# Performance work log

Measured on AMD Instinct MI355X. Metric: run time of the kernel, lower is better.

Reference implementation:

```python
import jax, jax.numpy as jnp
import numpy as np

B, N, DIM, H, DH, K = 4, 2048, 512, 6, 64, 16
KEEP_PROB = 0.9  # 1 - dropout_rate
LOG2PI = float(np.log(2.0 * np.pi))
LOG_PRIOR = float(np.log(1.0 / K))


def setup_inputs() -> dict:
    key = jax.random.key(0)
    ks = jax.random.split(key, 7)
    inputs_q = jax.random.normal(ks[0], (B, N, DIM), dtype=jnp.float32)
    # decoder-style causal mask, shape [B, 1, q_len, kv_len]
    causal = jnp.tril(jnp.ones((N, N), dtype=jnp.float32))
    mask = jnp.broadcast_to(causal[None, None], (B, 1, N, N))
    # dropout keep mask broadcast across the query dim: [B, H, 1, kv_len]
    keep = jax.random.bernoulli(ks[1], KEEP_PROB, (B, H, 1, N)).astype(jnp.float32)
    w_qkv = jax.random.normal(ks[2], (DIM, 3 * H * DH), dtype=jnp.float32) * 0.02
    w_out = jax.random.normal(ks[3], (H * DH, DIM), dtype=jnp.float32) * 0.02
    mu_lookup = jax.random.normal(ks[4], (K, DIM), dtype=jnp.float32)
    logvar_lookup = jax.random.normal(ks[5], (K, DIM), dtype=jnp.float32) * 0.1
    return {
        "inputs_q": inputs_q,
        "mask": mask,
        "keep": keep,
        "w_qkv": w_qkv,
        "w_out": w_out,
        "mu_lookup": mu_lookup,
        "logvar_lookup": logvar_lookup,
    }


def reference(inputs_q, mask, keep, w_qkv, w_out, mu_lookup, logvar_lookup):
    # --- MultiHeadDotProductAttention (self-attn path) ---
    qkv = (inputs_q @ w_qkv).reshape(B, N, 3, H, DH)  # [B,N,3,H,DH]
    q, k, v = qkv[:, :, 0], qkv[:, :, 1], qkv[:, :, 2]
    # bias: 0 where mask > 0, -1e10 elsewhere (note: no 1/sqrt(d) scaling, as in source)
    bias = jnp.where(mask > 0, 0.0, -1e10)
    attn_weights = jnp.einsum('bqhd,bkhd->bhqk', q, k) + bias  # [B,H,N,N]
    attn_weights = jax.nn.softmax(attn_weights, axis=-1)
    # broadcast dropout: mask shared across the query dim
    attn_weights = attn_weights * keep / KEEP_PROB
    attn_out = jnp.einsum('bhqk,bkhd->bqhd', attn_weights, v)
    attn_out = attn_out.reshape(B, N, H * DH) @ w_out  # [B,N,DIM]

    # --- GMM posterior approx q(y|x) ~= p(y|z) (approx_qy_x, vectorized over k) ---
    z = attn_out.mean(axis=1)  # pooled latent, [B,DIM]
    diff = z[:, None, :] - mu_lookup[None]  # [B,K,DIM]
    llh = -0.5 * jnp.sum(
        diff * diff / jnp.exp(logvar_lookup)[None] + logvar_lookup[None] + LOG2PI,
        axis=-1,
    )  # [B,K]
    logLogit_qy_x = llh + LOG_PRIOR
    qy_x = jax.nn.softmax(logLogit_qy_x, axis=1)  # [B,K]

    # combine mixture mean back in so both branches are live in one output
    return attn_out + (qy_x @ mu_lookup)[:, None, :]
```

## Files before the change

### kernel.cpp

```cpp
#include <hip/hip_runtime.h>
#include <cstdint>
#include <cstddef>

#define NH 6
#define NSEQ 2048
#define DIMD 512
#define BATCH 4
#define HD 384
#define LOG2PI_F 1.8378770664093453f

typedef __attribute__((ext_vector_type(8))) short short8;
typedef __attribute__((ext_vector_type(8))) unsigned short ushort8;
typedef __attribute__((ext_vector_type(4))) unsigned short ushort4v;
typedef __attribute__((ext_vector_type(4))) float floatx4;

__device__ inline unsigned short f2bf(float f){
  unsigned int u = __float_as_uint(f);
  u += 0x7FFFu + ((u>>16)&1u);
  return (unsigned short)(u>>16);
}

#define GLD16(gp, lp) __builtin_amdgcn_global_load_lds( \
  (const __attribute__((address_space(1))) void*)(gp), \
  (__attribute__((address_space(3))) void*)(lp), 16, 0, 0)

__global__ __launch_bounds__(256) void convert_x(
    const float* __restrict__ xq, unsigned short* __restrict__ xbf)
{
  int i = blockIdx.x*256 + threadIdx.x;
  floatx4 v = *(const floatx4*)(xq + (size_t)i*4);
  ushort4v r;
  #pragma unroll
  for(int j=0;j<4;j++) r[j] = f2bf(v[j]);
  *(ushort4v*)(xbf + (size_t)i*4) = r;
}

__global__ __launch_bounds__(256) void wtrans(
    const float* __restrict__ src, unsigned short* __restrict__ dst, int R, int C)
{
  __shared__ __attribute__((aligned(16))) unsigned short Ls[64*72];
  const int t = threadIdx.x;
  const int r = t>>2, c0 = (t&3)*16;
  const int d0 = blockIdx.y*64, n0 = blockIdx.x*64;
  #pragma unroll
  for (int j=0;j<16;j+=4){
    floatx4 v = *(const floatx4*)(src + (size_t)(d0+r)*C + n0 + c0 + j);
    #pragma unroll
    for(int jj=0;jj<4;jj++) Ls[r*72 + c0+j+jj] = f2bf(v[jj]);
  }
  __syncthreads();
  #pragma unroll
  for (int j=0;j<16;j+=8){
    ushort8 o;
    #pragma unroll
    for(int jj=0;jj<8;jj++) o[jj] = Ls[(c0+j+jj)*72 + r];
    *(ushort8*)(dst + (size_t)(n0+r)*R + d0 + c0 + j) = o;
  }
}

__global__ __launch_bounds__(256) void vtrans(
    const unsigned short* __restrict__ Vo, unsigned short* __restrict__ Vt)
{
  __shared__ __attribute__((aligned(16))) unsigned short Ls[64*72];
  const int t = threadIdx.x;
  const int r = t>>2, c0 = (t&3)*16;
  const int n0 = blockIdx.x*64, bh = blockIdx.y;
  #pragma unroll
  for (int j=0;j<16;j+=8)
    *(ushort8*)(Ls + r*72 + c0 + j) = *(const ushort8*)(Vo + ((size_t)bh*NSEQ + n0 + r)*64 + c0 + j);
  __syncthreads();
  #pragma unroll
  for (int j=0;j<16;j+=8){
    ushort8 o;
    #pragma unroll
    for(int jj=0;jj<8;jj++) o[jj] = Ls[(c0+j+jj)*72 + r];
    *(ushort8*)(Vt + ((size_t)bh*64 + r)*NSEQ + n0 + c0 + j) = o;
  }
}

__global__ __launch_bounds__(256) void gemm_qkv(
    const unsigned short* __restrict__ A,
    const unsigned short* __restrict__ Bt,
    const float* __restrict__ keep,
    unsigned short* __restrict__ Qo, unsigned short* __restrict__ Ko, unsigned short* __restrict__ Vo)
{
  __shared__ __attribute__((aligned(16))) unsigned short Cs[128*132];
  unsigned short* As = Cs;
  unsigned short* Bs = Cs + 128*64;
  const int tid = threadIdx.x;
  const int w = tid>>6, lane = tid&63;
  const int wr = w>>1, wc = w&1;
  const int quad = lane>>4, l16 = lane&15;
  const int tM = blockIdx.x*128, tN = blockIdx.y*128;
  const int r8 = lane>>3, c8 = (lane&7)*8;
  floatx4 acc[4][4];
  floatx4 zed = {0.f,0.f,0.f,0.f};
  #pragma unroll
  for (int i=0;i<4;i++)
    #pragma unroll
    for(int j=0;j<4;j++) acc[i][j] = zed;

  for (int k0=0; k0<512; k0+=64){
    #pragma unroll
    for (int i=0;i<4;i++){
      int row = w*32 + i*8;
      GLD16(A  + (size_t)(tM+row+r8)*512 + k0 + c8, As + row*64);
      GLD16(Bt + (size_t)(tN+row+r8)*512 + k0 + c8, Bs + row*64);
    }
    __syncthreads();
    #pragma unroll
    for (int kk=0; kk<64; kk+=32){
      short8 af[4], bf[4];
      #pragma unroll
      for(int mt=0;mt<4;mt++)
        af[mt] = *(const short8*)(As + (wr*64+mt*16+l16)*64 + kk + quad*8);
      #pragma unroll
      for(int nt=0;nt<4;nt++)
        bf[nt] = *(const short8*)(Bs + (wc*64+nt*16+l16)*64 + kk + quad*8);
      #pragma unroll
      for(int mt=0;mt<4;mt++)
        #pragma unroll
        for(int nt=0;nt<4;nt++)
          acc[mt][nt] = __builtin_amdgcn_mfma_f32_16x16x32_bf16(af[mt], bf[nt], acc[mt][nt], 0,0,0);
    }
    __syncthreads();
  }
  #pragma unroll
  for(int mt=0;mt<4;mt++)
    #pragma unroll
    for(int nt=0;nt<4;nt++)
      #pragma unroll
      for(int r=0;r<4;r++)
        Cs[(wr*64+mt*16+quad*4+r)*132 + wc*64+nt*16+l16] = f2bf(acc[mt][nt][r]);
  __syncthreads();
  const int row = tid>>1, colh = (tid&1)*64;
  const int gcol0 = tN + colh;
  const int t = gcol0/384, rem = gcol0 - t*384, h = rem>>6;
  const int grow = tM + row, b = grow>>11, n = grow & 2047;
  unsigned short* dst = (t==0 ? Qo : (t==1 ? Ko : Vo)) + ((size_t)((b*NH+h)*NSEQ+n))*64;
  bool vzero = false;
  if (t==2) vzero = (keep[(size_t)(b*NH+h)*NSEQ+n] < 0.5f);
  ushort8 zz;
  #pragma unroll
  for(int q2=0;q2<8;q2++) zz[q2]=0;
  #pragma unroll
  for(int j=0;j<8;j++){
    ushort8 v = *(const ushort8*)(Cs + row*132 + colh + j*8);
    *(ushort8*)(dst + j*8) = vzero ? zz : v;
  }
}

__global__ __launch_bounds__(64) void attn_kernel(
    const unsigned short* __restrict__ Qg, const unsigned short* __restrict__ Kg,
    const unsigned short* __restrict__ VtG,
    unsigned short* __restrict__ atp)
{
  __shared__ __attribute__((aligned(16))) unsigned short Ps[32*72];
  const int lane = threadIdx.x;
  const int quad = lane>>4, l16 = lane&15;
  const int bid = blockIdx.x;
  const int idx = bid>>3;
  const int bh  = (bid&7) + 8*(idx % 3);
  const int c   = 63 - idx/3;
  const int b = bh/NH, h = bh - b*NH;
  const unsigned short* Qb = Qg  + (size_t)bh*NSEQ*64;
  const unsigned short* Kb = Kg  + (size_t)bh*NSEQ*64;
  const unsigned short* Vb = VtG + (size_t)bh*64*NSEQ;
  const int q0 = c*32;
  const int nkt = (c>>1) + 1;

  short8 qf[2][2];
  #pragma unroll
  for(int mt=0;mt<2;mt++)
    #pragma unroll
    for(int kc=0;kc<2;kc++)
      qf[mt][kc] = *(const short8*)(Qb + (size_t)(q0+mt*16+l16)*64 + kc*32 + quad*8);

  short8 onesf;
  #pragma unroll
  for(int j=0;j<8;j++) onesf[j] = (short)0x3F80;

  floatx4 O[2][4];
  floatx4 accl[2];
  floatx4 zed = {0.f,0.f,0.f,0.f};
  #pragma unroll
  for(int mt=0;mt<2;mt++){
    #pragma unroll
    for(int dt=0;dt<4;dt++) O[mt][dt] = zed;
    accl[mt] = zed;
  }

  short8 kA[4][2], kB2[4][2];
  auto loadK = [&](int kt, short8 (&kf)[4][2]){
    const unsigned short* kp0 = Kb + (size_t)kt*64*64;
    #pragma unroll
    for(int nt=0;nt<4;nt++)
      #pragma unroll
      for(int kc=0;kc<2;kc++)
        kf[nt][kc] = *(const short8*)(kp0 + (size_t)(nt*16+l16)*64 + kc*32 + quad*8);
  };

  auto tile = [&](int kt, short8 (&kf)[4][2]){
    const int kB = kt*64;
    short8 vf[2][4];
    const unsigned short* vp0 = Vb + kB;
    #pragma unroll
    for(int kh=0;kh<2;kh++)
      #pragma unroll
      for(int dt=0;dt<4;dt++)
        vf[kh][dt] = *(const short8*)(vp0 + (size_t)(dt*16+l16)*NSEQ + kh*32 + quad*8);

    floatx4 sacc[2][4];
    floatx4 m12 = {-12.f,-12.f,-12.f,-12.f};
    #pragma unroll
    for(int mt=0;mt<2;mt++)
      #pragma unroll
      for(int nt=0;nt<4;nt++) sacc[mt][nt] = m12;
    #pragma unroll
    for(int mt=0;mt<2;mt++)
      #pragma unroll
      for(int nt=0;nt<4;nt++)
        #pragma unroll
        for(int kc=0;kc<2;kc++)
          sacc[mt][nt] = __builtin_amdgcn_mfma_f32_16x16x32_bf16(qf[mt][kc], kf[nt][kc], sacc[mt][nt], 0,0,0);

    const bool dia = (kt == nkt-1);
    #pragma unroll
    for(int mt=0;mt<2;mt++){
      #pragma unroll
      for(int nt=0;nt<4;nt++){
        int key = kB + nt*16 + l16;
        #pragma unroll
        for(int r=0;r<4;r++){
          float p = __expf(sacc[mt][nt][r]);
          if (dia) p = (key <= q0 + mt*16 + quad*4 + r) ? p : 0.f;
          Ps[(mt*16+quad*4+r)*72 + nt*16 + l16] = f2bf(p);
        }
      }
    }
    #pragma unroll
    for(int kh=0;kh<2;kh++){
      #pragma unroll
      for(int mt=0;mt<2;mt++){
        short8 pf = *(const short8*)(Ps + (mt*16+l16)*72 + kh*32 + quad*8);
        accl[mt] = __builtin_amdgcn_mfma_f32_16x16x32_bf16(pf, onesf, accl[mt], 0,0,0);
        #pragma unroll
        for(int dt=0;dt<4;dt++)
          O[mt][dt] = __builtin_amdgcn_mfma_f32_16x16x32_bf16(pf, vf[kh][dt], O[mt][dt], 0,0,0);
      }
    }
  };

  loadK(0, kA);
  int kt = 0;
  while (true){
    loadK(kt+1 < nkt ? kt+1 : kt, kB2);
    tile(kt, kA);
    kt++; if (kt >= nkt) break;
    loadK(kt+1 < nkt ? kt+1 : kt, kA);
    tile(kt, kB2);
    kt++; if (kt >= nkt) break;
  }

  #pragma unroll
  for(int mt=0;mt<2;mt++)
    #pragma unroll
    for(int r=0;r<4;r++){
      float sc2 = (1.0f/0.9f) / accl[mt][r];
      #pragma unroll
      for(int dt=0;dt<4;dt++)
        Ps[(mt*16+quad*4+r)*72 + dt*16 + l16] = f2bf(O[mt][dt][r]*sc2);
    }
  const int orow = lane>>1, ohalf = (lane&1)*32;
  const int q = q0 + orow;
  unsigned short* dstp = atp + ((size_t)(b*NSEQ+q))*HD + h*64 + ohalf;
  #pragma unroll
  for(int j=0;j<4;j++)
    *(ushort8*)(dstp + j*8) = *(const ushort8*)(Ps + orow*72 + ohalf + j*8);
}

__global__ __launch_bounds__(256) void gemm_proj(
    const unsigned short* __restrict__ A,
    const unsigned short* __restrict__ Bt,
    float* __restrict__ out,
    float* __restrict__ z)
{
  __shared__ __attribute__((aligned(16))) unsigned short As[128*64];
  __shared__ __attribute__((aligned(16))) unsigned short Bs[128*64];
  const int tid = threadIdx.x;
  const int w = tid>>6, lane = tid&63;
  const int wr = w>>1, wc = w&1;
  const int quad = lane>>4, l16 = lane&15;
  const int tM = blockIdx.x*128, tN = blockIdx.y*128;
  const int r8 = lane>>3, c8 = (lane&7)*8;
  floatx4 acc[4][4];
  floatx4 zed = {0.f,0.f,0.f,0.f};
  #pragma unroll
  for (int i=0;i<4;i++)
    #pragma unroll
    for(int j=0;j<4;j++) acc[i][j] = zed;

  for (int k0=0; k0<384; k0+=64){
    #pragma unroll
    for (int i=0;i<4;i++){
      int row = w*32 + i*8;
      GLD16(A  + (size_t)(tM+row+r8)*384 + k0 + c8, As + row*64);
      GLD16(Bt + (size_t)(tN+row+r8)*384 + k0 + c8, Bs + row*64);
    }
    __syncthreads();
    #pragma unroll
    for (int kk=0; kk<64; kk+=32){
      short8 af[4], bf[4];
      #pragma unroll
      for(int mt=0;mt<4;mt++)
        af[mt] = *(const short8*)(As + (wr*64+mt*16+l16)*64 + kk + quad*8);
      #pragma unroll
      for(int nt=0;nt<4;nt++)
        bf[nt] = *(const short8*)(Bs + (wc*64+nt*16+l16)*64 + kk + quad*8);
      #pragma unroll
      for(int mt=0;mt<4;mt++)
        #pragma unroll
        for(int nt=0;nt<4;nt++)
          acc[mt][nt] = __builtin_amdgcn_mfma_f32_16x16x32_bf16(af[mt], bf[nt], acc[mt][nt], 0,0,0);
    }
    __syncthreads();
  }
  #pragma unroll
  for(int mt=0;mt<4;mt++){
    int grow = tM + wr*64 + mt*16 + quad*4;
    #pragma unroll
    for(int nt=0;nt<4;nt++){
      int gcol = tN + wc*64 + nt*16 + l16;
      #pragma unroll
      for(int r=0;r<4;r++)
        out[(size_t)(grow+r)*512 + gcol] = acc[mt][nt][r];
    }
  }
  #pragma unroll
  for(int nt=0;nt<4;nt++){
    float s = 0.f;
    #pragma unroll
    for(int mt=0;mt<4;mt++)
      #pragma unroll
      for(int r=0;r<4;r++) s += acc[mt][nt][r];
    s += __shfl_xor(s, 16, 64);
    s += __shfl_xor(s, 32, 64);
    if (quad == 0){
      int gcol = tN + wc*64 + nt*16 + l16;
      atomicAdd(&z[(tM>>11)*DIMD + gcol], s);
    }
  }
}

__global__ __launch_bounds__(256) void gmm_kernel(
    const float* __restrict__ z, const float* __restrict__ mu,
    const float* __restrict__ lv, float* __restrict__ c)
{
  __shared__ float sh[16];
  __shared__ float qy[16];
  int tid = threadIdx.x;
  int k = tid>>4, li = tid&15;
  int b = blockIdx.x;
  float part = 0.f;
  for(int d=li; d<DIMD; d+=16){
    float zz = z[b*DIMD+d] * (1.0f/2048.0f);
    float m = mu[k*DIMD+d], l = lv[k*DIMD+d];
    float diff = zz - m;
    part += diff*diff*__expf(-l) + l + LOG2PI_F;
  }
  #pragma unroll
  for(int off=8;off>=1;off>>=1) part += __shfl_xor(part, off, 64);
  if (li==0) sh[k] = part;
  __syncthreads();
  if (tid<16){
    float logit = -0.5f*sh[tid];
    float mx = logit;
    #pragma unroll
    for(int off=8;off>=1;off>>=1) mx = fmaxf(mx, __shfl_xor(mx, off, 64));
    float e = __expf(logit-mx);
    float se = e;
    #pragma unroll
    for(int off=8;off>=1;off>>=1) se += __shfl_xor(se, off, 64);
    qy[tid] = e/se;
  }
  __syncthreads();
  for(int d=tid; d<DIMD; d+=256){
    float accv = 0.f;
    #pragma unroll
    for(int kk=0;kk<16;kk++) accv += qy[kk]*mu[kk*DIMD+d];
    c[b*DIMD+d] = accv;
  }
}

__global__ __launch_bounds__(256) void final_add(
    float* __restrict__ out, const float* __restrict__ c)
{
  size_t i = ((size_t)blockIdx.x*256 + threadIdx.x)*4;
  int d = (int)(i & 511);
  int b = (int)(i >> 20);
  floatx4 a = *(const floatx4*)(out + i);
  floatx4 cc = *(const floatx4*)(c + b*DIMD + d);
  *(floatx4*)(out + i) = a + cc;
}

extern "C" void kernel_launch(void* const* d_in, const int* in_sizes, int n_in,
                              void* d_out, int out_size, void* d_ws, size_t ws_size,
                              hipStream_t stream) {
  const float* inputs_q = (const float*)d_in[0];
  const float* keep  = (const float*)d_in[2];
  const float* w_qkv = (const float*)d_in[3];
  const float* w_out = (const float*)d_in[4];
  const float* mu    = (const float*)d_in[5];
  const float* lv    = (const float*)d_in[6];
  float* out = (float*)d_out;
  char* ws = (char*)d_ws;
  size_t off = 0;
  auto alloc = [&](size_t bytes){ void* p = ws + off; off += (bytes + 255) & ~(size_t)255; return p; };
  unsigned short* Qb  = (unsigned short*)alloc((size_t)24*2048*64*2);
  unsigned short* Kb  = (unsigned short*)alloc((size_t)24*2048*64*2);
  unsigned short* Vo  = (unsigned short*)alloc((size_t)24*2048*64*2);
  unsigned short* Vt  = (unsigned short*)alloc((size_t)24*64*2048*2);
  unsigned short* xbf = (unsigned short*)alloc((size_t)8192*512*2);
  unsigned short* wqT = (unsigned short*)alloc((size_t)1152*512*2);
  unsigned short* woT = (unsigned short*)alloc((size_t)512*384*2);
  unsigned short* atp = (unsigned short*)alloc((size_t)8192*384*2);
  float* z  = (float*)alloc((size_t)4*512*4);
  float* c  = (float*)alloc((size_t)4*512*4);

  hipMemsetAsync(z, 0, 4*512*4, stream);
  convert_x<<<4096, 256, 0, stream>>>(inputs_q, xbf);
  wtrans<<<dim3(18,8), 256, 0, stream>>>(w_qkv, wqT, 512, 1152);
  wtrans<<<dim3(8,6),  256, 0, stream>>>(w_out, woT, 384, 512);
  gemm_qkv<<<dim3(64,9), 256, 0, stream>>>(xbf, wqT, keep, Qb, Kb, Vo);
  vtrans<<<dim3(32,24), 256, 0, stream>>>(Vo, Vt);
  attn_kernel<<<1536, 64, 0, stream>>>(Qb, Kb, Vt, atp);
  gemm_proj<<<dim3(64,4), 256, 0, stream>>>(atp, woT, out, z);
  gmm_kernel<<<4, 256, 0, stream>>>(z, mu, lv, c);
  final_add<<<4096, 256, 0, stream>>>(out, c);
}
```

Measured before the change: 246.1 us.

## Split attention key tiles across four waves and reduce partial outputs in LDS

The attention kernel now runs four waves per block, each handling every fourth key tile for the same 32-query block. Per-wave partial O and row-sum accumulators are written to shared memory and summed before normalisation and the bf16 store. This shortens the serial key loop of each block for long causal rows and improves load balance. In exchange it adds an LDS reduction, two barriers and larger shared memory, and short rows leave some waves idle.

Result: slower. 265.8 us (+8.0%).

```diff
diff --git a/kernel.cpp b/kernel.cpp
--- a/kernel.cpp
+++ b/kernel.cpp
@@ -150,13 +150,17 @@
   }
 }
 
-__global__ __launch_bounds__(64) void attn_kernel(
+__global__ __launch_bounds__(256, 4) void attn_kernel(
     const unsigned short* __restrict__ Qg, const unsigned short* __restrict__ Kg,
     const unsigned short* __restrict__ VtG,
     unsigned short* __restrict__ atp)
 {
-  __shared__ __attribute__((aligned(16))) unsigned short Ps[32*72];
-  const int lane = threadIdx.x;
+  __shared__ __attribute__((aligned(16))) char sm[4*32*68*4 + 4*32*4];
+  const int tid = threadIdx.x;
+  const int w = tid>>6, lane = tid&63;
+  unsigned short* Ps = (unsigned short*)sm + w*(32*72);
+  float* Oc   = (float*)sm;
+  float* accs = (float*)(sm + 4*32*68*4);
   const int quad = lane>>4, l16 = lane&15;
   const int bid = blockIdx.x;
   const int idx = bid>>3;
@@ -251,32 +255,57 @@
     }
   };
 
-  loadK(0, kA);
-  int kt = 0;
-  while (true){
-    loadK(kt+1 < nkt ? kt+1 : kt, kB2);
-    tile(kt, kA);
-    kt++; if (kt >= nkt) break;
-    loadK(kt+1 < nkt ? kt+1 : kt, kA);
-    tile(kt, kB2);
-    kt++; if (kt >= nkt) break;
-  }
-
-  #pragma unroll
-  for(int mt=0;mt<2;mt++)
-    #pragma unroll
-    for(int r=0;r<4;r++){
-      float sc2 = (1.0f/0.9f) / accl[mt][r];
+  int kt = w;
+  if (kt < nkt){
+    loadK(kt, kA);
+    while (true){
+      int nx = kt + 4;
+      loadK(nx < nkt ? nx : kt, kB2);
+      tile(kt, kA);
+      kt = nx; if (kt >= nkt) break;
+      nx = kt + 4;
+      loadK(nx < nkt ? nx : kt, kA);
+      tile(kt, kB2);
+      kt = nx; if (kt >= nkt) break;
+    }
+  }
+
+  __syncthreads();
+  {
+    float* Ow = Oc + w*(32*68);
+    #pragma unroll
+    for(int mt=0;mt<2;mt++){
       #pragma unroll
       for(int dt=0;dt<4;dt++)
-        Ps[(mt*16+quad*4+r)*72 + dt*16 + l16] = f2bf(O[mt][dt][r]*sc2);
-    }
-  const int orow = lane>>1, ohalf = (lane&1)*32;
-  const int q = q0 + orow;
-  unsigned short* dstp = atp + ((size_t)(b*NSEQ+q))*HD + h*64 + ohalf;
-  #pragma unroll
-  for(int j=0;j<4;j++)
-    *(ushort8*)(dstp + j*8) = *(const ushort8*)(Ps + orow*72 + ohalf + j*8);
+        #pragma unroll
+        for(int r=0;r<4;r++)
+          Ow[(mt*16+quad*4+r)*68 + dt*16 + l16] = O[mt][dt][r];
+      if (l16 == 0){
+        #pragma unroll
+        for(int r=0;r<4;r++)
+          accs[w*32 + mt*16+quad*4+r] = accl[mt][r];
+      }
+    }
+  }
+  __syncthreads();
+
+  const int orow = tid>>3, oc0 = (tid&7)*8;
+  float as = accs[0*32+orow] + accs[1*32+orow] + accs[2*32+orow] + accs[3*32+orow];
+  float sc2 = (1.0f/0.9f) / as;
+  float vsum[8];
+  #pragma unroll
+  for(int j=0;j<8;j++) vsum[j] = 0.f;
+  #pragma unroll
+  for(int s=0;s<4;s++){
+    const float* p = Oc + s*(32*68) + orow*68 + oc0;
+    #pragma unroll
+    for(int j=0;j<8;j++) vsum[j] += p[j];
+  }
+  ushort8 o;
+  #pragma unroll
+  for(int j=0;j<8;j++) o[j] = f2bf(vsum[j]*sc2);
+  unsigned short* dstp = atp + ((size_t)(b*NSEQ + q0 + orow))*HD + h*64 + oc0;
+  *(ushort8*)dstp = o;
 }
 
 __global__ __launch_bounds__(256) void gemm_proj(
@@ -433,7 +462,7 @@
   wtrans<<<dim3(8,6),  256, 0, stream>>>(w_out, woT, 384, 512);
   gemm_qkv<<<dim3(64,9), 256, 0, stream>>>(xbf, wqT, keep, Qb, Kb, Vo);
   vtrans<<<dim3(32,24), 256, 0, stream>>>(Vo, Vt);
-  attn_kernel<<<1536, 64, 0, stream>>>(Qb, Kb, Vt, atp);
+  attn_kernel<<<1536, 256, 0, stream>>>(Qb, Kb, Vt, atp);
   gemm_proj<<<dim3(64,4), 256, 0, stream>>>(atp, woT, out, z);
   gmm_kernel<<<4, 256, 0, stream>>>(z, mu, lv, c);
   final_add<<<4096, 256, 0, stream>>>(out, c);
```
